# Optimization experiments

Hardware: AMD Instinct MI355X
Metric: run time of the kernel (lower is better)

## Reference

```python
import jax, jax.numpy as jnp
import numpy as np

N = 50000
E = 800000
D_IN = 128
D_HID = 256


def setup_inputs() -> dict:
    key = jax.random.key(0)
    ks = jax.random.split(key, 9)
    x = jax.random.normal(ks[0], (N, D_IN), dtype=jnp.float32)
    edge_index = jax.random.randint(ks[1], (2, E), 0, N, dtype=jnp.int64)
    edge_weight = jax.random.uniform(ks[2], (E,), dtype=jnp.float32)
    # GCNConv params (lin: y = x @ W.T, plus bias added after aggregation)
    W1 = jax.random.normal(ks[3], (D_HID, D_IN), dtype=jnp.float32) / np.sqrt(D_IN)
    b1 = jnp.zeros((D_HID,), dtype=jnp.float32)
    W2 = jax.random.normal(ks[4], (D_IN, D_HID), dtype=jnp.float32) / np.sqrt(D_HID)
    b2 = jnp.zeros((D_IN,), dtype=jnp.float32)
    gamma = jnp.ones((D_IN,), dtype=jnp.float32)
    beta = jnp.zeros((D_IN,), dtype=jnp.float32)
    return {"x": x, "edge_index": edge_index, "edge_weight": edge_weight,
            "W1": W1, "b1": b1, "W2": W2, "b2": b2,
            "gamma": gamma, "beta": beta}


def _gcn_norm(edge_index, edge_weight, n_nodes):
    # add self loops with weight 1.0 (PyG gcn_norm default)
    loop = jnp.arange(n_nodes, dtype=edge_index.dtype)
    src = jnp.concatenate([edge_index[0], loop])
    dst = jnp.concatenate([edge_index[1], loop])
    w = jnp.concatenate([edge_weight, jnp.ones((n_nodes,), edge_weight.dtype)])
    # symmetric normalization: deg over target index
    deg = jax.ops.segment_sum(w, dst, num_segments=n_nodes)
    dinv = jnp.where(deg > 0, jax.lax.rsqrt(deg), 0.0)
    norm = dinv[src] * w * dinv[dst]
    return src, dst, norm


def _gcn_conv(x, src, dst, norm, W, b, n_nodes):
    h = x @ W.T                                    # [N, out]
    msg = h[src] * norm[:, None]                   # gather + scale [E+N, out]
    out = jax.ops.segment_sum(msg, dst, num_segments=n_nodes)
    return out + b


def reference(x, edge_index, edge_weight, W1, b1, W2, b2, gamma, beta):
    n_nodes = x.shape[0]
    src, dst, norm = _gcn_norm(edge_index, edge_weight, n_nodes)
    h = _gcn_conv(x, src, dst, norm, W1, b1, n_nodes)
    h = jax.nn.relu(h)
    h = _gcn_conv(h, src, dst, norm, W2, b2, n_nodes)
    # LayerNorm over last dim
    mu = jnp.mean(h, axis=-1, keepdims=True)
    var = jnp.mean(jnp.square(h - mu), axis=-1, keepdims=True)
    h = (h - mu) * jax.lax.rsqrt(var + 1e-5) * gamma + beta
    return h
```

## Files before the change

### kernel.cpp

```cpp
#include <hip/hip_runtime.h>

typedef unsigned short ushort_t;
typedef __attribute__((ext_vector_type(8))) short short8;
typedef __attribute__((ext_vector_type(4))) float float4v;

#define MAXDEG 48

__device__ inline float b2f(ushort_t u) {
    unsigned x = ((unsigned)u) << 16;
    return __builtin_bit_cast(float, x);
}
__device__ inline ushort_t f2b(float f) {
    unsigned x = __builtin_bit_cast(unsigned, f);
    unsigned r = (x + 0x7fffu + ((x >> 16) & 1u)) >> 16;
    return (ushort_t)r;
}

__device__ inline void load_edge(const int* __restrict__ ei, int e, int E,
                                 int& s, int& d) {
    int ec = min(e, E - 1);
    int2 c64 = ((const int2*)ei)[ec];
    unsigned long long m = __ballot(c64.y != 0);
    if (m != 0ull) {
        s = ei[ec];
        d = ei[(size_t)E + ec];
    } else {
        s = c64.x;
        d = ((const int2*)ei)[(size_t)E + ec].x;
    }
}


__global__ __launch_bounds__(256) void k_mega(const int* __restrict__ ei,
                                              const float* __restrict__ w,
                                              const float* __restrict__ x,
                                              const float* __restrict__ W1,
                                              const float* __restrict__ W2,
                                              unsigned* packed,
                                              unsigned* __restrict__ edata,
                                              ushort_t* __restrict__ xb,
                                              ushort_t* __restrict__ W1b,
                                              ushort_t* __restrict__ W2b,
                                              int E, int Nn, int gE, int gX) {
    int b = blockIdx.x;
    if (b < gE) {
        int e = b * 256 + threadIdx.x;
        int s, d;
        load_edge(ei, e, E, s, d);
        if (e < E) {
            if ((unsigned)s < (unsigned)Nn && (unsigned)d < (unsigned)Nn) {
                float wv = w[e];
                unsigned fx = (unsigned)(wv * 65536.0f + 0.5f);
                unsigned old = atomicAdd(packed + d, (1u << 22) | fx);
                int r = (int)(old >> 22);
                if (r < MAXDEG) {
                    unsigned wq = (unsigned)(wv * 32768.0f + 0.5f);
                    wq = min(wq, 32767u);
                    edata[(size_t)d * MAXDEG + r] = ((unsigned)s << 15) | wq;
                }
            }
        }
    } else if (b < gE + gX) {
        int i = (b - gE) * 256 + threadIdx.x;
        if (i < Nn * 32) {
            float4v v = ((const float4v*)x)[i];
            ushort4 o;
            o.x = f2b(v[0]); o.y = f2b(v[1]); o.z = f2b(v[2]); o.w = f2b(v[3]);
            ((ushort4*)xb)[i] = o;
        }
    } else {
        int i = (b - gE - gX) * 256 + threadIdx.x;
        if (i < 32768) W1b[i] = f2b(W1[i]);
        else if (i < 65536) W2b[i - 32768] = f2b(W2[i - 32768]);
    }
}


__global__ __launch_bounds__(256) void k_dinv(const unsigned* __restrict__ packed,
                                              float* __restrict__ dinv, int Nn) {
    int i = blockIdx.x * 256 + threadIdx.x;
    if (i < Nn) {
        float wsum = (float)(packed[i] & 0x3FFFFFu) * (1.0f / 65536.0f);
        dinv[i] = rsqrtf(1.0f + wsum);
    }
}


__device__ inline void agg_edges(const ushort_t* __restrict__ src,
                                 const unsigned* __restrict__ ed, int n,
                                 const float* __restrict__ dinv,
                                 int hl, int p, float* a) {
    int i = 0;
    for (; i + 7 < n; i += 8) {
#pragma unroll
        for (int j = 0; j < 4; ++j) {
            int idx = i + p + 2 * j;
            unsigned e2 = ed[idx];
            int sN = (int)(e2 >> 15);
            float nw = dinv[sN] * (float)(e2 & 0x7FFFu) * (1.0f / 32768.0f);
            ushort4 q = ((const ushort4*)(src + (size_t)sN * 128))[hl];
            a[0] += b2f(q.x) * nw; a[1] += b2f(q.y) * nw;
            a[2] += b2f(q.z) * nw; a[3] += b2f(q.w) * nw;
        }
    }
    for (; i < n; i += 2) {
        int idx = i + p;
        int ic = min(idx, n - 1);
        unsigned e2 = ed[ic];
        int sN = (int)(e2 >> 15);
        float nw = (idx < n)
                       ? dinv[sN] * (float)(e2 & 0x7FFFu) * (1.0f / 32768.0f)
                       : 0.f;
        ushort4 q = ((const ushort4*)(src + (size_t)sN * 128))[hl];
        a[0] += b2f(q.x) * nw; a[1] += b2f(q.y) * nw;
        a[2] += b2f(q.z) * nw; a[3] += b2f(q.w) * nw;
    }
}


__global__ __launch_bounds__(256) void k_agg1(const ushort_t* __restrict__ xb,
                                              const unsigned* __restrict__ packed,
                                              const unsigned* __restrict__ edata,
                                              const float* __restrict__ dinv,
                                              ushort_t* __restrict__ ax, int Nn) {
    int v = (blockIdx.x * blockDim.x + threadIdx.x) >> 6;
    int lane = threadIdx.x & 63;
    if (v >= Nn) return;
    int hl = lane & 31, p = lane >> 5;
    float dv = dinv[v];
    float a[4] = {0.f, 0.f, 0.f, 0.f};
    if (p == 0) {
        ushort4 pq = ((const ushort4*)(xb + (size_t)v * 128))[hl];
        a[0] = b2f(pq.x) * dv; a[1] = b2f(pq.y) * dv;
        a[2] = b2f(pq.z) * dv; a[3] = b2f(pq.w) * dv;
    }
    int n = min((int)(packed[v] >> 22), MAXDEG);
    agg_edges(xb, edata + (size_t)v * MAXDEG, n, dinv, hl, p, a);
#pragma unroll
    for (int j = 0; j < 4; ++j) {
        a[j] *= dv;
        a[j] += __shfl_xor(a[j], 32);
    }
    if (p == 0) {
        ushort4 o;
        o.x = f2b(a[0]); o.y = f2b(a[1]); o.z = f2b(a[2]); o.w = f2b(a[3]);
        ((ushort4*)(ax + (size_t)v * 128))[hl] = o;
    }
}


__global__ __launch_bounds__(256, 2) void k_gemm_fused(const ushort_t* __restrict__ ax,
                                                       const ushort_t* __restrict__ W1b,
                                                       const float* __restrict__ b1v,
                                                       const ushort_t* __restrict__ W2b,
                                                       ushort_t* __restrict__ h2, int Nn) {
    __shared__ ushort_t tile[64][264];
    int tid = threadIdx.x, wid = tid >> 6, lane = tid & 63;
    int m = lane & 15, q = lane >> 4;
    int blk = blockIdx.x * 64;

    short8 wf[4][4];
#pragma unroll
    for (int nt = 0; nt < 4; ++nt) {
        const ushort_t* wb = W1b + (size_t)(wid * 64 + nt * 16 + m) * 128 + q * 8;
#pragma unroll
        for (int kt = 0; kt < 4; ++kt) wf[nt][kt] = *(const short8*)(wb + kt * 32);
    }
    short8 af[4][4];
#pragma unroll
    for (int mi = 0; mi < 4; ++mi) {
        int arow = blk + mi * 16 + m;
        bool rv = arow < Nn;
        const ushort_t* ab = ax + (size_t)arow * 128 + q * 8;
#pragma unroll
        for (int kt = 0; kt < 4; ++kt)
            af[mi][kt] = rv ? *(const short8*)(ab + kt * 32) : (short8)0;
    }

    float4v acc1[4][4];
#pragma unroll
    for (int mi = 0; mi < 4; ++mi)
#pragma unroll
        for (int nt = 0; nt < 4; ++nt) acc1[mi][nt] = (float4v){0.f, 0.f, 0.f, 0.f};

#pragma unroll
    for (int kt = 0; kt < 4; ++kt)
#pragma unroll
        for (int mi = 0; mi < 4; ++mi)
#pragma unroll
            for (int nt = 0; nt < 4; ++nt)
                acc1[mi][nt] = __builtin_amdgcn_mfma_f32_16x16x32_bf16(
                    af[mi][kt], wf[nt][kt], acc1[mi][nt], 0, 0, 0);

#pragma unroll
    for (int nt = 0; nt < 4; ++nt) {
        int col = wid * 64 + nt * 16 + m;
        float bb = b1v[col];
#pragma unroll
        for (int mi = 0; mi < 4; ++mi) {
#pragma unroll
            for (int r = 0; r < 4; ++r) {
                float v = acc1[mi][nt][r] + bb;
                v = v > 0.f ? v : 0.f;
                tile[mi * 16 + q * 4 + r][col] = f2b(v);
            }
        }
    }
    __syncthreads();

    short8 w2f[2][8];
#pragma unroll
    for (int n2 = 0; n2 < 2; ++n2) {
        const ushort_t* wb = W2b + (size_t)(wid * 32 + n2 * 16 + m) * 256 + q * 8;
#pragma unroll
        for (int kt = 0; kt < 8; ++kt) w2f[n2][kt] = *(const short8*)(wb + kt * 32);
    }

    float4v acc2[4][2];
#pragma unroll
    for (int mi = 0; mi < 4; ++mi)
#pragma unroll
        for (int n2 = 0; n2 < 2; ++n2) acc2[mi][n2] = (float4v){0.f, 0.f, 0.f, 0.f};

#pragma unroll
    for (int kt = 0; kt < 8; ++kt) {
#pragma unroll
        for (int mi = 0; mi < 4; ++mi) {
            short8 a2 = *(const short8*)&tile[mi * 16 + m][kt * 32 + q * 8];
#pragma unroll
            for (int n2 = 0; n2 < 2; ++n2)
                acc2[mi][n2] = __builtin_amdgcn_mfma_f32_16x16x32_bf16(
                    a2, w2f[n2][kt], acc2[mi][n2], 0, 0, 0);
        }
    }

#pragma unroll
    for (int mi = 0; mi < 4; ++mi) {
#pragma unroll
        for (int n2 = 0; n2 < 2; ++n2) {
            int col = wid * 32 + n2 * 16 + m;
#pragma unroll
            for (int r = 0; r < 4; ++r) {
                int row = blk + mi * 16 + q * 4 + r;
                if (row < Nn) h2[(size_t)row * 128 + col] = f2b(acc2[mi][n2][r]);
            }
        }
    }
}


__global__ __launch_bounds__(256) void k_agg2_ln(const ushort_t* __restrict__ h2,
                                                 const unsigned* __restrict__ packed,
                                                 const unsigned* __restrict__ edata,
                                                 const float* __restrict__ dinv,
                                                 const float* __restrict__ b2v,
                                                 const float* __restrict__ gv,
                                                 const float* __restrict__ bev,
                                                 float* __restrict__ out, int Nn) {
    int v = (blockIdx.x * blockDim.x + threadIdx.x) >> 6;
    int lane = threadIdx.x & 63;
    if (v >= Nn) return;
    int hl = lane & 31, p = lane >> 5;
    float dv = dinv[v];
    float a[4] = {0.f, 0.f, 0.f, 0.f};
    if (p == 0) {
        ushort4 pq = ((const ushort4*)(h2 + (size_t)v * 128))[hl];
        a[0] = b2f(pq.x) * dv; a[1] = b2f(pq.y) * dv;
        a[2] = b2f(pq.z) * dv; a[3] = b2f(pq.w) * dv;
    }
    int n = min((int)(packed[v] >> 22), MAXDEG);
    agg_edges(h2, edata + (size_t)v * MAXDEG, n, dinv, hl, p, a);
#pragma unroll
    for (int j = 0; j < 4; ++j) {
        a[j] *= dv;
        a[j] += __shfl_xor(a[j], 32);
    }

    int d0 = hl * 4;
#pragma unroll
    for (int j = 0; j < 4; ++j) a[j] += b2v[d0 + j];

    float ssum = a[0] + a[1] + a[2] + a[3];
    float ssq = a[0] * a[0] + a[1] * a[1] + a[2] * a[2] + a[3] * a[3];
#pragma unroll
    for (int off = 1; off < 64; off <<= 1) {
        ssum += __shfl_xor(ssum, off);
        ssq += __shfl_xor(ssq, off);
    }
    float mu = ssum * (1.0f / 256.0f);
    float var = ssq * (1.0f / 256.0f) - mu * mu;
    float r = rsqrtf(var + 1e-5f);
    if (p == 0) {
        float4v o;
#pragma unroll
        for (int j = 0; j < 4; ++j)
            o[j] = (a[j] - mu) * r * gv[d0 + j] + bev[d0 + j];
        ((float4v*)(out + (size_t)v * 128))[hl] = o;
    }
}


extern "C" void kernel_launch(void* const* d_in, const int* in_sizes, int n_in,
                              void* d_out, int out_size, void* d_ws, size_t ws_size,
                              hipStream_t stream) {
    const float* x   = (const float*)d_in[0];
    const int*   ei  = (const int*)d_in[1];
    const float* ew  = (const float*)d_in[2];
    const float* W1  = (const float*)d_in[3];
    const float* b1v = (const float*)d_in[4];
    const float* W2  = (const float*)d_in[5];
    const float* b2v = (const float*)d_in[6];
    const float* gv  = (const float*)d_in[7];
    const float* bev = (const float*)d_in[8];
    float* out = (float*)d_out;

    const int Nn = in_sizes[0] / 128;
    const int E  = in_sizes[2];

    char* base = (char*)d_ws;
    size_t off = 0;
    auto alloc = [&](size_t bytes) {
        char* p = base + off;
        off = (off + bytes + 255) & ~(size_t)255;
        return p;
    };
    unsigned* packed = (unsigned*)alloc((size_t)Nn * 4);
    float*    dinv   = (float*)alloc((size_t)Nn * 4);
    unsigned* edata  = (unsigned*)alloc((size_t)Nn * MAXDEG * 4);
    ushort_t* xb     = (ushort_t*)alloc((size_t)Nn * 128 * 2);
    ushort_t* h2     = (ushort_t*)alloc((size_t)Nn * 128 * 2);
    ushort_t* W1b    = (ushort_t*)alloc(32768 * 2);
    ushort_t* W2b    = (ushort_t*)alloc(32768 * 2);
    ushort_t* ax     = (ushort_t*)d_out;
    (void)ws_size; (void)n_in; (void)out_size;

    int gE = (E + 255) / 256;
    int gX = (Nn * 32 + 255) / 256;
    int gW = (Nn + 3) / 4;
    int gG = (Nn + 63) / 64;
    int gD = (Nn + 255) / 256;

    hipMemsetAsync(packed, 0, (size_t)Nn * 4, stream);
    k_mega<<<gE + gX + 256, 256, 0, stream>>>(ei, ew, x, W1, W2, packed, edata,
                                              xb, W1b, W2b, E, Nn, gE, gX);
    k_dinv<<<gD, 256, 0, stream>>>(packed, dinv, Nn);
    k_agg1<<<gW, 256, 0, stream>>>(xb, packed, edata, dinv, ax, Nn);
    k_gemm_fused<<<gG, 256, 0, stream>>>(ax, W1b, b1v, W2b, h2, Nn);
    k_agg2_ln<<<gW, 256, 0, stream>>>(h2, packed, edata, dinv, b2v, gv, bev, out, Nn);
}
```

Baseline: 246.4 us.

## Pad per-node atomic counters to 64B stride and batch gather loads in aggregation

```diff
diff --git a/kernel.cpp b/kernel.cpp
--- a/kernel.cpp
+++ b/kernel.cpp
@@ -5,6 +5,7 @@
 typedef __attribute__((ext_vector_type(4))) float float4v;
 
 #define MAXDEG 48
+#define CSTRIDE 16
 
 __device__ inline float b2f(ushort_t u) {
     unsigned x = ((unsigned)u) << 16;
@@ -51,7 +52,8 @@
             if ((unsigned)s < (unsigned)Nn && (unsigned)d < (unsigned)Nn) {
                 float wv = w[e];
                 unsigned fx = (unsigned)(wv * 65536.0f + 0.5f);
-                unsigned old = atomicAdd(packed + d, (1u << 22) | fx);
+                unsigned old = atomicAdd(packed + (size_t)d * CSTRIDE,
+                                         (1u << 22) | fx);
                 int r = (int)(old >> 22);
                 if (r < MAXDEG) {
                     unsigned wq = (unsigned)(wv * 32768.0f + 0.5f);
@@ -80,7 +82,7 @@
                                               float* __restrict__ dinv, int Nn) {
     int i = blockIdx.x * 256 + threadIdx.x;
     if (i < Nn) {
-        float wsum = (float)(packed[i] & 0x3FFFFFu) * (1.0f / 65536.0f);
+        float wsum = (float)(packed[(size_t)i * CSTRIDE] & 0x3FFFFFu) * (1.0f / 65536.0f);
         dinv[i] = rsqrtf(1.0f + wsum);
     }
 }
@@ -91,16 +93,40 @@
                                  const float* __restrict__ dinv,
                                  int hl, int p, float* a) {
     int i = 0;
+    for (; i + 15 < n; i += 16) {
+        unsigned e2[8];
+#pragma unroll
+        for (int j = 0; j < 8; ++j) e2[j] = ed[i + p + 2 * j];
+        ushort4 q[8];
+        float nw[8];
+#pragma unroll
+        for (int j = 0; j < 8; ++j) {
+            int sN = (int)(e2[j] >> 15);
+            q[j] = ((const ushort4*)(src + (size_t)sN * 128))[hl];
+            nw[j] = dinv[sN] * (float)(e2[j] & 0x7FFFu) * (1.0f / 32768.0f);
+        }
+#pragma unroll
+        for (int j = 0; j < 8; ++j) {
+            a[0] += b2f(q[j].x) * nw[j]; a[1] += b2f(q[j].y) * nw[j];
+            a[2] += b2f(q[j].z) * nw[j]; a[3] += b2f(q[j].w) * nw[j];
+        }
+    }
     for (; i + 7 < n; i += 8) {
+        unsigned e2[4];
+#pragma unroll
+        for (int j = 0; j < 4; ++j) e2[j] = ed[i + p + 2 * j];
+        ushort4 q[4];
+        float nw[4];
 #pragma unroll
         for (int j = 0; j < 4; ++j) {
-            int idx = i + p + 2 * j;
-            unsigned e2 = ed[idx];
-            int sN = (int)(e2 >> 15);
-            float nw = dinv[sN] * (float)(e2 & 0x7FFFu) * (1.0f / 32768.0f);
-            ushort4 q = ((const ushort4*)(src + (size_t)sN * 128))[hl];
-            a[0] += b2f(q.x) * nw; a[1] += b2f(q.y) * nw;
-            a[2] += b2f(q.z) * nw; a[3] += b2f(q.w) * nw;
+            int sN = (int)(e2[j] >> 15);
+            q[j] = ((const ushort4*)(src + (size_t)sN * 128))[hl];
+            nw[j] = dinv[sN] * (float)(e2[j] & 0x7FFFu) * (1.0f / 32768.0f);
+        }
+#pragma unroll
+        for (int j = 0; j < 4; ++j) {
+            a[0] += b2f(q[j].x) * nw[j]; a[1] += b2f(q[j].y) * nw[j];
+            a[2] += b2f(q[j].z) * nw[j]; a[3] += b2f(q[j].w) * nw[j];
         }
     }
     for (; i < n; i += 2) {
@@ -134,7 +160,7 @@
         a[0] = b2f(pq.x) * dv; a[1] = b2f(pq.y) * dv;
         a[2] = b2f(pq.z) * dv; a[3] = b2f(pq.w) * dv;
     }
-    int n = min((int)(packed[v] >> 22), MAXDEG);
+    int n = min((int)(packed[(size_t)v * CSTRIDE] >> 22), MAXDEG);
     agg_edges(xb, edata + (size_t)v * MAXDEG, n, dinv, hl, p, a);
 #pragma unroll
     for (int j = 0; j < 4; ++j) {
@@ -268,7 +294,7 @@
         a[0] = b2f(pq.x) * dv; a[1] = b2f(pq.y) * dv;
         a[2] = b2f(pq.z) * dv; a[3] = b2f(pq.w) * dv;
     }
-    int n = min((int)(packed[v] >> 22), MAXDEG);
+    int n = min((int)(packed[(size_t)v * CSTRIDE] >> 22), MAXDEG);
     agg_edges(h2, edata + (size_t)v * MAXDEG, n, dinv, hl, p, a);
 #pragma unroll
     for (int j = 0; j < 4; ++j) {
@@ -324,7 +350,7 @@
         off = (off + bytes + 255) & ~(size_t)255;
         return p;
     };
-    unsigned* packed = (unsigned*)alloc((size_t)Nn * 4);
+    unsigned* packed = (unsigned*)alloc((size_t)Nn * CSTRIDE * 4);
     float*    dinv   = (float*)alloc((size_t)Nn * 4);
     unsigned* edata  = (unsigned*)alloc((size_t)Nn * MAXDEG * 4);
     ushort_t* xb     = (ushort_t*)alloc((size_t)Nn * 128 * 2);
@@ -340,7 +366,7 @@
     int gG = (Nn + 63) / 64;
     int gD = (Nn + 255) / 256;
 
-    hipMemsetAsync(packed, 0, (size_t)Nn * 4, stream);
+    hipMemsetAsync(packed, 0, (size_t)Nn * CSTRIDE * 4, stream);
     k_mega<<<gE + gX + 256, 256, 0, stream>>>(ei, ew, x, W1, W2, packed, edata,
                                               xb, W1b, W2b, E, Nn, gE, gX);
     k_dinv<<<gD, 256, 0, stream>>>(packed, dinv, Nn);
```

Measured after the change: 244.4 us. About the same (-0.8%).
